# Kernel optimization log

Measured on AMD Instinct MI355X. Metric: run time of the kernel, lower is better.

Reference implementation:

```python
import math
import jax, jax.numpy as jnp
import numpy as np
from jax.scipy.special import xlogy, gammaln


def get_positional_embed(seq_len, feature_size):
    # Enformer-style relative positional basis over distances [-(L-1), L-1].
    distances = jnp.arange(-seq_len + 1, seq_len, dtype=jnp.float32)  # [2L-1]
    n = feature_size // 6
    absd = jnp.abs(distances)[:, None]  # [2L-1, 1]

    # exponential basis
    max_range = math.log(seq_len) / math.log(2.0)
    half_life = 2.0 ** jnp.linspace(3.0, max_range, n)  # [n]
    feat_exp = jnp.exp(-math.log(2.0) / half_life[None, :] * absd)

    # central mask basis
    center_widths = 2.0 ** jnp.arange(1, n + 1, dtype=jnp.float32) - 1.0
    feat_cm = (center_widths[None, :] > absd).astype(jnp.float32)

    # gamma pdf basis
    stddev = seq_len / (2.0 * n)
    start_mean = seq_len / n
    mean = jnp.linspace(start_mean, float(seq_len), n)[None, :]
    conc = (mean / stddev) ** 2
    rate = mean / stddev ** 2
    log_unnorm = xlogy(conc - 1.0, absd) - rate * absd
    log_norm = gammaln(conc) - conc * jnp.log(rate)
    probs = jnp.exp(log_unnorm - log_norm) + 1e-8
    feat_gamma = probs / jnp.max(probs, axis=-1, keepdims=True)

    emb = jnp.concatenate([feat_exp, feat_cm, feat_gamma], axis=-1)  # [2L-1, 3n]
    emb = jnp.concatenate([emb, jnp.sign(distances)[:, None] * emb], axis=-1)  # [2L-1, 6n]
    return emb


def relative_shift(x):
    # x: [B, H, Q, 2K-1] -> [B, H, Q, K]
    b, h, t1, t2m1 = x.shape
    x = jnp.pad(x, ((0, 0), (0, 0), (0, 0), (1, 0)))  # [B,H,Q,2K]
    t2 = t2m1 + 1
    x = x.reshape(b, h, t2, t1)
    x = x[:, :, 1:, :]
    x = x.reshape(b, h, t1, t2 - 1)
    return x[..., : (t2 + 1) // 2]


def setup_inputs() -> dict:
    key = jax.random.key(0)
    ks = jax.random.split(key, 9)
    B, L, D = 2, 1024, 1024
    H, Dk, Dv = 8, 128, 128
    R = 192  # n_rel_pos_features
    sq = math.sqrt(2.0 / (D + Dk))
    sv = math.sqrt(2.0 / (D + Dv))
    return {
        "q": jax.random.normal(ks[0], (B, L, D), jnp.float32),
        "w_qs": jax.random.normal(ks[1], (D, H * Dk), jnp.float32) * sq,
        "w_ks": jax.random.normal(ks[2], (D, H * Dk), jnp.float32) * sq,
        "w_vs": jax.random.normal(ks[3], (D, H * Dv), jnp.float32) * sv,
        "w_rel_pos_k": jax.random.normal(ks[4], (R, H * Dk), jnp.float32) * 0.05,
        "rel_embed_bias": jax.random.normal(ks[5], (1, H, 1, Dk), jnp.float32),
        "rel_pos_bias": jax.random.normal(ks[6], (1, H, 1, Dk), jnp.float32),
        "w_out": jax.random.normal(ks[7], (H * Dv, D), jnp.float32) * 0.02,
        "b_out": jax.random.normal(ks[8], (D,), jnp.float32) * 0.02,
    }


def reference(q, w_qs, w_ks, w_vs, w_rel_pos_k, rel_embed_bias, rel_pos_bias, w_out, b_out):
    B, L, _ = q.shape
    H, Dk = rel_embed_bias.shape[1], rel_embed_bias.shape[3]
    Dv = w_vs.shape[1] // H
    scale = Dk ** (-0.5)

    Q = (q @ w_qs).reshape(B, L, H, Dk).transpose(0, 2, 1, 3) * scale  # [B,H,L,Dk]
    K = (q @ w_ks).reshape(B, L, H, Dk).transpose(0, 2, 1, 3)
    V = (q @ w_vs).reshape(B, L, H, Dv).transpose(0, 2, 1, 3)

    attn = jnp.einsum('bnqd,bnkd->bnqk', Q + rel_embed_bias, K)

    positions = get_positional_embed(L, w_rel_pos_k.shape[0])  # [2L-1, R]
    rel_k = (positions @ w_rel_pos_k).reshape(-1, H, Dk).transpose(1, 0, 2)  # [H,2L-1,Dk]
    attn_pos = jnp.einsum('bnqd,nkd->bnqk', Q + rel_pos_bias, rel_k)  # [B,H,L,2L-1]
    attn_pos = relative_shift(attn_pos)  # [B,H,L,L]

    a = jax.nn.softmax(attn + attn_pos, axis=-1)
    out = jnp.einsum('bnqk,bnkd->bnqd', a, V)
    out = out.transpose(0, 2, 1, 3).reshape(B, L, H * Dv)
    return out @ w_out + b_out
```

## Files before the change

### kernel.cpp

```cpp
#include <hip/hip_runtime.h>
#include <hip/hip_fp16.h>

typedef __attribute__((ext_vector_type(8))) _Float16 f16x8;
typedef __attribute__((ext_vector_type(4))) float f32x4;

#define MFMA16(a, b, c) __builtin_amdgcn_mfma_f32_16x16x32_f16((a), (b), (c), 0, 0, 0)

__device__ __forceinline__ unsigned short f2h(float f) {
  __half h = __float2half(f);
  return __half_as_ushort(h);
}

__device__ __forceinline__ void gll16(const void* g, void* l) {
  __builtin_amdgcn_global_load_lds(
      (const __attribute__((address_space(1))) unsigned int*)g,
      (__attribute__((address_space(3))) unsigned int*)l, 16, 0, 0);
}

__global__ void cvt_f16_kernel(const float* __restrict__ X, unsigned short* __restrict__ Y) {
  size_t i = ((size_t)blockIdx.x * blockDim.x + threadIdx.x) * 4;
  float4 v = *reinterpret_cast<const float4*>(X + i);
  ushort4 o;
  o.x = f2h(v.x); o.y = f2h(v.y); o.z = f2h(v.z); o.w = f2h(v.w);
  *reinterpret_cast<ushort4*>(Y + i) = o;
}

__global__ void transpose_w4_kernel(const float* __restrict__ W0, const float* __restrict__ W1,
                                    const float* __restrict__ W2, const float* __restrict__ W3,
                                    unsigned short* __restrict__ T0, unsigned short* __restrict__ T1,
                                    unsigned short* __restrict__ T2, unsigned short* __restrict__ T3) {
  __shared__ float tile[32][33];
  int z = blockIdx.z;
  const float* W = (z == 0) ? W0 : ((z == 1) ? W1 : ((z == 2) ? W2 : W3));
  unsigned short* WT = (z == 0) ? T0 : ((z == 1) ? T1 : ((z == 2) ? T2 : T3));
  int c0 = blockIdx.x * 32, r0 = blockIdx.y * 32;
  int tx = threadIdx.x, ty = threadIdx.y;
#pragma unroll
  for (int i = 0; i < 32; i += 8)
    tile[ty + i][tx] = W[(size_t)(r0 + ty + i) * 1024 + c0 + tx];
  __syncthreads();
#pragma unroll
  for (int i = 0; i < 32; i += 8)
    WT[(size_t)(c0 + ty + i) * 1024 + r0 + tx] = f2h(tile[tx][ty + i]);
}

__global__ void transpose_wr_kernel(const float* __restrict__ W, unsigned short* __restrict__ WT) {
  __shared__ float tile[32][33];
  int c0 = blockIdx.x * 32, r0 = blockIdx.y * 32;
  int tx = threadIdx.x, ty = threadIdx.y;
#pragma unroll
  for (int i = 0; i < 32; i += 8)
    tile[ty + i][tx] = W[(size_t)(r0 + ty + i) * 1024 + c0 + tx];
  __syncthreads();
#pragma unroll
  for (int i = 0; i < 32; i += 8)
    WT[(size_t)(c0 + ty + i) * 192 + r0 + tx] = f2h(tile[tx][ty + i]);
}

__global__ void posembed_kernel(unsigned short* __restrict__ pos) {
  int grp = (blockIdx.x * blockDim.x + threadIdx.x) >> 5;
  int j = threadIdx.x & 31;
  if (grp >= 2048) return;
  unsigned short* row = pos + (size_t)grp * 192;
  if (grp == 2047) {
#pragma unroll
    for (int t = 0; t < 6; ++t) row[t * 32 + j] = 0;
    return;
  }
  float dist = (float)grp - 1023.0f;
  float absd = fabsf(dist);
  float jp = (float)(j + 1);
  float hl = exp2f(3.0f + (float)j * (7.0f / 31.0f));
  float fe = exp2f(-absd / hl);
  float cw = exp2f(jp) - 1.0f;
  float fc = (cw > absd) ? 1.0f : 0.0f;
  float conc = 4.0f * jp * jp;
  float rate = 0.125f * jp;
  float lu = (conc - 1.0f) * logf(absd) - rate * absd;
  float ln_ = lgammaf(conc) - conc * logf(rate);
  float p = expf(lu - ln_) + 1e-8f;
  float mp = p;
#pragma unroll
  for (int off = 16; off >= 1; off >>= 1) mp = fmaxf(mp, __shfl_xor(mp, off));
  float gm = p / mp;
  unsigned short e = f2h(fe), c = f2h(fc), gg = f2h(gm);
  row[j] = e; row[32 + j] = c; row[64 + j] = gg;
  unsigned short se, sc, sg;
  if (dist > 0.0f)      { se = e; sc = c; sg = gg; }
  else if (dist < 0.0f) { se = (unsigned short)(e ^ 0x8000u);
                          sc = (unsigned short)(c ^ 0x8000u);
                          sg = (unsigned short)(gg ^ 0x8000u); }
  else                  { se = 0; sc = 0; sg = 0; }
  row[96 + j] = se; row[128 + j] = sc; row[160 + j] = sg;
}

__global__ __launch_bounds__(256) void gemm16_kernel(
    const unsigned short* __restrict__ A,
    const unsigned short* __restrict__ BT0, const unsigned short* __restrict__ BT1,
    const unsigned short* __restrict__ BT2,
    unsigned short* __restrict__ D0, unsigned short* __restrict__ D1,
    unsigned short* __restrict__ D2,
    float* __restrict__ C32, const float* __restrict__ bias,
    int M, int N, int K) {
  __shared__ unsigned short As[128][64];
  __shared__ unsigned short Bs[128][64];
  const unsigned short* BT = (blockIdx.z == 0) ? BT0 : ((blockIdx.z == 1) ? BT1 : BT2);
  unsigned short* D = (blockIdx.z == 0) ? D0 : ((blockIdx.z == 1) ? D1 : D2);

  int tid = threadIdx.x, wave = tid >> 6, lane = tid & 63;
  int g = lane >> 4, r16 = lane & 15;
  int wr = wave >> 1, wc = wave & 1;
  int m0 = blockIdx.x * 128, n0 = blockIdx.y * 128;
  int srow = wave * 32 + (lane >> 3);
  int scb = lane & 7;

  f32x4 acc[4][4] = {};

  for (int k0 = 0; k0 < K; k0 += 64) {
    __syncthreads();
#pragma unroll
    for (int i = 0; i < 4; ++i) {
      int row = srow + i * 8;
      int cb = scb ^ (row & 7);
      gll16(A + (size_t)(m0 + row) * K + k0 + cb * 8, &As[row][scb * 8]);
      gll16(BT + (size_t)(n0 + row) * K + k0 + cb * 8, &Bs[row][scb * 8]);
    }
    asm volatile("s_waitcnt vmcnt(0)" ::: "memory");
    __syncthreads();

    f16x8 af[2][4], bfr[2][4];
#pragma unroll
    for (int kf = 0; kf < 2; ++kf) {
#pragma unroll
      for (int mt = 0; mt < 4; ++mt) {
        int R = wr * 64 + mt * 16 + r16;
        af[kf][mt] = *reinterpret_cast<const f16x8*>(&As[R][(((kf * 4 + g)) ^ (R & 7)) * 8]);
      }
#pragma unroll
      for (int nt = 0; nt < 4; ++nt) {
        int R = wc * 64 + nt * 16 + r16;
        bfr[kf][nt] = *reinterpret_cast<const f16x8*>(&Bs[R][(((kf * 4 + g)) ^ (R & 7)) * 8]);
      }
    }
#pragma unroll
    for (int kf = 0; kf < 2; ++kf)
#pragma unroll
      for (int mt = 0; mt < 4; ++mt)
#pragma unroll
        for (int nt = 0; nt < 4; ++nt)
          acc[mt][nt] = MFMA16(af[kf][mt], bfr[kf][nt], acc[mt][nt]);
  }

#pragma unroll
  for (int nt = 0; nt < 4; ++nt) {
    int col = n0 + wc * 64 + nt * 16 + r16;
    float bv = (C32 && bias) ? bias[col] : 0.0f;
#pragma unroll
    for (int mt = 0; mt < 4; ++mt) {
      int rowb = m0 + wr * 64 + mt * 16 + g * 4;
      if (C32) {
#pragma unroll
        for (int rg = 0; rg < 4; ++rg)
          C32[(size_t)(rowb + rg) * N + col] = acc[mt][nt][rg] + bv;
      } else {
#pragma unroll
        for (int rg = 0; rg < 4; ++rg)
          D[(size_t)(rowb + rg) * N + col] = f2h(acc[mt][nt][rg]);
      }
    }
  }
}

__global__ void vt_prep_kernel(const unsigned short* __restrict__ Vh, unsigned short* __restrict__ Vt) {
  __shared__ unsigned short tile[32][34];
  int bh = blockIdx.z;
  int b = bh >> 3, h = bh & 7;
  int l0 = blockIdx.x * 32, n0 = blockIdx.y * 32;
  int tx = threadIdx.x, ty = threadIdx.y;
#pragma unroll
  for (int i = 0; i < 32; i += 8)
    tile[ty + i][tx] = Vh[(size_t)(b * 1024 + l0 + ty + i) * 1024 + h * 128 + n0 + tx];
  __syncthreads();
#pragma unroll
  for (int i = 0; i < 32; i += 8)
    Vt[(size_t)bh * 131072 + (size_t)(n0 + ty + i) * 1024 + l0 + tx] = tile[tx][ty + i];
}

__global__ __launch_bounds__(256) void attn_kernel(
    const unsigned short* __restrict__ Qh, const unsigned short* __restrict__ Kh,
    const unsigned short* __restrict__ Vt, const unsigned short* __restrict__ relkh,
    const float* __restrict__ eb, const float* __restrict__ pb,
    unsigned short* __restrict__ Opart, float* __restrict__ mlpart) {
  __shared__ unsigned short Ks[2][32 * 128];
  __shared__ unsigned short Rs[128 * 128];
  __shared__ unsigned short Vs[2][128][40];
  __shared__ unsigned short Ps[4][16][42];

  int tid = threadIdx.x;
  int wave = tid >> 6, lane = tid & 63;
  int g = lane >> 4, r16 = lane & 15;
  int ks = blockIdx.y;
  int bh = blockIdx.z;
  int b = bh >> 3, h = bh & 7;
  int q0 = blockIdx.x * 64;
  int q0w = q0 + wave * 16;
  const float scale = 0.0883883476483184f;

  f16x8 qa[4], qbv[4];
  {
    int qrow = b * 1024 + q0w + r16;
    const unsigned short* qp = Qh + (size_t)qrow * 1024 + h * 128;
    const float* ebp = eb + h * 128;
    const float* pbp = pb + h * 128;
#pragma unroll
    for (int kf = 0; kf < 4; ++kf) {
      int dbase = kf * 32 + g * 8;
      uint4 qv = *reinterpret_cast<const uint4*>(qp + dbase);
      const __half* hv = reinterpret_cast<const __half*>(&qv);
      float4 e0 = *reinterpret_cast<const float4*>(ebp + dbase);
      float4 e1 = *reinterpret_cast<const float4*>(ebp + dbase + 4);
      float4 c0 = *reinterpret_cast<const float4*>(pbp + dbase);
      float4 c1 = *reinterpret_cast<const float4*>(pbp + dbase + 4);
      float ev[8] = {e0.x, e0.y, e0.z, e0.w, e1.x, e1.y, e1.z, e1.w};
      float bv[8] = {c0.x, c0.y, c0.z, c0.w, c1.x, c1.y, c1.z, c1.w};
      unsigned short ta[8], tb[8];
#pragma unroll
      for (int i = 0; i < 8; ++i) {
        float s = __half2float(hv[i]) * scale;
        ta[i] = f2h(s + ev[i]);
        tb[i] = f2h(s + bv[i]);
      }
      qa[kf] = *reinterpret_cast<f16x8*>(ta);
      qbv[kf] = *reinterpret_cast<f16x8*>(tb);
    }
  }

  float m_run[4], l_part[4];
#pragma unroll
  for (int rg = 0; rg < 4; ++rg) { m_run[rg] = -1e30f; l_part[rg] = 0.0f; }
  f32x4 o_acc[8] = {};

  const unsigned short* KB = Kh + ((size_t)b * 1024) * 1024 + h * 128;
  const unsigned short* VB = Vt + (size_t)bh * 131072;
  const unsigned short* RB = relkh + h * 128;
  int wb = 48 - wave * 16;

  const int t0 = ks * 16, t1 = t0 + 16;
  const int rb0 = 960 + t0 * 32 - q0;

  uint4 va, vb2;
#pragma unroll
  for (int i = 0; i < 2; ++i) {
    int j = i * 256 + tid;
    int row = j >> 4, s = j & 15, c = s ^ (row & 7);
    gll16(KB + (size_t)(t0 * 32 + row) * 1024 + c * 8, &Ks[t0 & 1][(row * 16 + s) * 8]);
  }
#pragma unroll
  for (int i = 0; i < 6; ++i) {
    int j = i * 256 + tid;
    int row = rb0 + (j >> 4);
    int s = j & 15, c = s ^ (row & 7);
    gll16(RB + (size_t)row * 1024 + c * 8, &Rs[(((row & 127) * 16) + s) * 8]);
  }
  {
    const unsigned short* src = VB + (size_t)(tid >> 1) * 1024 + t0 * 32 + (tid & 1) * 16;
    va = *reinterpret_cast<const uint4*>(src);
    vb2 = *reinterpret_cast<const uint4*>(src + 8);
  }

  for (int t = t0; t < t1; ++t) {
    int cur = t & 1;
    asm volatile("s_waitcnt vmcnt(0)" ::: "memory");
    {
      int rr = tid >> 1, cc = (tid & 1) * 16;
      *reinterpret_cast<uint4*>(&Vs[cur][rr][cc]) = va;
      *reinterpret_cast<uint4*>(&Vs[cur][rr][cc + 8]) = vb2;
    }
    __syncthreads();

    if (t + 1 < t1) {
      int nk0 = (t + 1) * 32;
#pragma unroll
      for (int i = 0; i < 2; ++i) {
        int j = i * 256 + tid;
        int row = j >> 4, s = j & 15, c = s ^ (row & 7);
        gll16(KB + (size_t)(nk0 + row) * 1024 + c * 8, &Ks[(t + 1) & 1][(row * 16 + s) * 8]);
      }
      int rnew = rb0 + 96 + (t - t0) * 32;
#pragma unroll
      for (int i = 0; i < 2; ++i) {
        int j = i * 256 + tid;
        int row = rnew + (j >> 4);
        int s = j & 15, c = s ^ (row & 7);
        gll16(RB + (size_t)row * 1024 + c * 8, &Rs[(((row & 127) * 16) + s) * 8]);
      }
      const unsigned short* src = VB + (size_t)(tid >> 1) * 1024 + nk0 + (tid & 1) * 16;
      va = *reinterpret_cast<const uint4*>(src);
      vb2 = *reinterpret_cast<const uint4*>(src + 8);
    }

    int k0 = t * 32;
    int rbt = rb0 + (t - t0) * 32;
    f32x4 s0 = {0.f, 0.f, 0.f, 0.f}, s1 = {0.f, 0.f, 0.f, 0.f};
    f32x4 w0 = {0.f, 0.f, 0.f, 0.f}, w1 = {0.f, 0.f, 0.f, 0.f}, w2 = {0.f, 0.f, 0.f, 0.f};
#pragma unroll
    for (int kf = 0; kf < 4; ++kf) {
      int sl = kf * 4 + g;
      int x = sl ^ (r16 & 7);
      f16x8 kb0 = *reinterpret_cast<const f16x8*>(&Ks[cur][(r16 * 16 + x) * 8]);
      f16x8 kb1 = *reinterpret_cast<const f16x8*>(&Ks[cur][((16 + r16) * 16 + x) * 8]);
      s0 = MFMA16(qa[kf], kb0, s0);
      s1 = MFMA16(qa[kf], kb1, s1);
      int R0 = rbt + wb + r16, R1 = R0 + 16, R2 = R0 + 32;
      f16x8 rb_0 = *reinterpret_cast<const f16x8*>(&Rs[((R0 & 127) * 16 + (sl ^ (R0 & 7))) * 8]);
      f16x8 rb_1 = *reinterpret_cast<const f16x8*>(&Rs[((R1 & 127) * 16 + (sl ^ (R1 & 7))) * 8]);
      f16x8 rb_2 = *reinterpret_cast<const f16x8*>(&Rs[((R2 & 127) * 16 + (sl ^ (R2 & 7))) * 8]);
      w0 = MFMA16(qbv[kf], rb_0, w0);
      w1 = MFMA16(qbv[kf], rb_1, w1);
      w2 = MFMA16(qbv[kf], rb_2, w2);
    }

    float sv[2][4];
#pragma unroll
    for (int rg = 0; rg < 4; ++rg) {
      int qp = g * 4 + rg;
      int idx = r16 + 15 - qp;
      int srcl = (lane & 48) | (idx & 15);
      float a0 = __shfl(w0[rg], srcl);
      float a1 = __shfl(w1[rg], srcl);
      float a2 = __shfl(w2[rg], srcl);
      bool lo = idx < 16;
      sv[0][rg] = s0[rg] + (lo ? a0 : a1);
      sv[1][rg] = s1[rg] + (lo ? a1 : a2);
    }

    float d = -1e30f;
#pragma unroll
    for (int rg = 0; rg < 4; ++rg)
      d = fmaxf(d, fmaxf(sv[0][rg], sv[1][rg]) - m_run[rg]);
    if (!__all(d <= 8.0f)) {
#pragma unroll
      for (int rg = 0; rg < 4; ++rg) {
        float mx = fmaxf(sv[0][rg], sv[1][rg]);
#pragma unroll
        for (int off = 8; off >= 1; off >>= 1) mx = fmaxf(mx, __shfl_xor(mx, off));
        float mnew = fmaxf(m_run[rg], mx);
        float scl = __expf(m_run[rg] - mnew);
        l_part[rg] *= scl;
#pragma unroll
        for (int nf = 0; nf < 8; ++nf) o_acc[nf][rg] *= scl;
        m_run[rg] = mnew;
      }
    }
#pragma unroll
    for (int rg = 0; rg < 4; ++rg) {
      float e0 = __expf(sv[0][rg] - m_run[rg]);
      float e1 = __expf(sv[1][rg] - m_run[rg]);
      l_part[rg] += e0 + e1;
      Ps[wave][g * 4 + rg][r16] = f2h(e0);
      Ps[wave][g * 4 + rg][16 + r16] = f2h(e1);
    }
    f16x8 pf = *reinterpret_cast<const f16x8*>(&Ps[wave][r16][g * 8]);
#pragma unroll
    for (int nf = 0; nf < 8; ++nf) {
      f16x8 vb = *reinterpret_cast<const f16x8*>(&Vs[cur][nf * 16 + r16][g * 8]);
      o_acc[nf] = MFMA16(pf, vb, o_acc[nf]);
    }
  }

  float l_run[4];
#pragma unroll
  for (int rg = 0; rg < 4; ++rg) {
    float rs = l_part[rg];
#pragma unroll
    for (int off = 8; off >= 1; off >>= 1) rs += __shfl_xor(rs, off);
    l_run[rg] = rs;
  }

  size_t slice = (size_t)(ks * 16 + bh);
#pragma unroll
  for (int rg = 0; rg < 4; ++rg) {
    unsigned short* op = Opart + (slice * 1024 + q0w + g * 4 + rg) * 128;
#pragma unroll
    for (int nf = 0; nf < 8; ++nf) op[nf * 16 + r16] = f2h(o_acc[nf][rg]);
  }
  if (r16 == 0) {
#pragma unroll
    for (int rg = 0; rg < 4; ++rg) {
      float2 ml = {m_run[rg], l_run[rg]};
      *reinterpret_cast<float2*>(mlpart + (slice * 1024 + q0w + g * 4 + rg) * 2) = ml;
    }
  }
}

__global__ void combine_kernel(const unsigned short* __restrict__ Opart,
                               const float* __restrict__ mlpart,
                               unsigned short* __restrict__ attnO) {
  int idx = blockIdx.x * 256 + threadIdx.x;
  int d4 = (idx & 31) * 4;
  int qq = (idx >> 5) & 1023;
  int bh = idx >> 15;
  float2 ml[2];
  float m = -1e30f;
#pragma unroll
  for (int s = 0; s < 2; ++s) {
    ml[s] = *reinterpret_cast<const float2*>(mlpart + (((size_t)(s * 16 + bh)) * 1024 + qq) * 2);
    m = fmaxf(m, ml[s].x);
  }
  float num0 = 0.f, num1 = 0.f, num2 = 0.f, num3 = 0.f, den = 0.f;
#pragma unroll
  for (int s = 0; s < 2; ++s) {
    float w = __expf(ml[s].x - m);
    den += w * ml[s].y;
    ushort4 ov = *reinterpret_cast<const ushort4*>(
        Opart + (((size_t)(s * 16 + bh)) * 1024 + qq) * 128 + d4);
    num0 += w * __half2float(__ushort_as_half(ov.x));
    num1 += w * __half2float(__ushort_as_half(ov.y));
    num2 += w * __half2float(__ushort_as_half(ov.z));
    num3 += w * __half2float(__ushort_as_half(ov.w));
  }
  float inv = 1.0f / den;
  ushort4 o;
  o.x = f2h(num0 * inv); o.y = f2h(num1 * inv);
  o.z = f2h(num2 * inv); o.w = f2h(num3 * inv);
  int b = bh >> 3, h = bh & 7;
  *reinterpret_cast<ushort4*>(attnO + ((size_t)(b * 1024 + qq)) * 1024 + h * 128 + d4) = o;
}

extern "C" void kernel_launch(void* const* d_in, const int* in_sizes, int n_in,
                              void* d_out, int out_size, void* d_ws, size_t ws_size,
                              hipStream_t stream) {
  const float* q      = (const float*)d_in[0];
  const float* w_qs   = (const float*)d_in[1];
  const float* w_ks   = (const float*)d_in[2];
  const float* w_vs   = (const float*)d_in[3];
  const float* w_rel  = (const float*)d_in[4];
  const float* ebias  = (const float*)d_in[5];
  const float* pbias  = (const float*)d_in[6];
  const float* w_out  = (const float*)d_in[7];
  const float* b_out  = (const float*)d_in[8];
  float* out = (float*)d_out;

  char* ws = (char*)d_ws;
  const size_t MB = 1u << 20;
  unsigned short* Xh    = (unsigned short*)(ws + 0 * MB);
  unsigned short* WqsT  = (unsigned short*)(ws + 4 * MB);
  unsigned short* WksT  = (unsigned short*)(ws + 6 * MB);
  unsigned short* WvsT  = (unsigned short*)(ws + 8 * MB);
  unsigned short* WoutT = (unsigned short*)(ws + 10 * MB);
  unsigned short* WrelT = (unsigned short*)(ws + 12 * MB);
  unsigned short* pos   = (unsigned short*)(ws + 13 * MB);
  unsigned short* Qh    = (unsigned short*)(ws + 14 * MB);
  unsigned short* Kh    = (unsigned short*)(ws + 18 * MB);
  unsigned short* Vh    = (unsigned short*)(ws + 22 * MB);
  unsigned short* relkh = (unsigned short*)(ws + 26 * MB);
  unsigned short* Vt    = (unsigned short*)(ws + 30 * MB);
  unsigned short* attnO = (unsigned short*)(ws + 34 * MB);
  unsigned short* Opart = (unsigned short*)(ws + 38 * MB);
  float* mlpart         = (float*)(ws + 50 * MB);

  cvt_f16_kernel<<<2048, 256, 0, stream>>>(q, Xh);
  transpose_w4_kernel<<<dim3(32, 32, 4), dim3(32, 8), 0, stream>>>(
      w_qs, w_ks, w_vs, w_out, WqsT, WksT, WvsT, WoutT);
  transpose_wr_kernel<<<dim3(32, 6), dim3(32, 8), 0, stream>>>(w_rel, WrelT);
  posembed_kernel<<<256, 256, 0, stream>>>(pos);

  gemm16_kernel<<<dim3(16, 8, 3), 256, 0, stream>>>(Xh, WqsT, WksT, WvsT,
                                                    Qh, Kh, Vh,
                                                    nullptr, nullptr, 2048, 1024, 1024);
  gemm16_kernel<<<dim3(16, 8, 1), 256, 0, stream>>>(pos, WrelT, WrelT, WrelT,
                                                    relkh, relkh, relkh,
                                                    nullptr, nullptr, 2048, 1024, 192);

  vt_prep_kernel<<<dim3(32, 4, 16), dim3(32, 8), 0, stream>>>(Vh, Vt);

  attn_kernel<<<dim3(16, 2, 16), 256, 0, stream>>>(Qh, Kh, Vt, relkh, ebias, pbias,
                                                   Opart, mlpart);
  combine_kernel<<<2048, 256, 0, stream>>>(Opart, mlpart, attnO);

  gemm16_kernel<<<dim3(16, 8, 1), 256, 0, stream>>>(attnO, WoutT, WoutT, WoutT,
                                                    nullptr, nullptr, nullptr,
                                                    out, b_out, 2048, 1024, 1024);
}
```

Before: 118.7 us.

## Merge rel-pos GEMM into QKV launch, split-K output GEMM, swizzle attention blocks

```diff
diff --git a/kernel.cpp b/kernel.cpp
--- a/kernel.cpp
+++ b/kernel.cpp
@@ -95,17 +95,20 @@
 }
 
 __global__ __launch_bounds__(256) void gemm16_kernel(
-    const unsigned short* __restrict__ A,
+    const unsigned short* __restrict__ A, const unsigned short* __restrict__ A3,
     const unsigned short* __restrict__ BT0, const unsigned short* __restrict__ BT1,
-    const unsigned short* __restrict__ BT2,
+    const unsigned short* __restrict__ BT2, const unsigned short* __restrict__ BT3,
     unsigned short* __restrict__ D0, unsigned short* __restrict__ D1,
-    unsigned short* __restrict__ D2,
-    float* __restrict__ C32, const float* __restrict__ bias,
-    int M, int N, int K) {
+    unsigned short* __restrict__ D2, unsigned short* __restrict__ D3,
+    int Kmain, int K3) {
   __shared__ unsigned short As[128][64];
   __shared__ unsigned short Bs[128][64];
-  const unsigned short* BT = (blockIdx.z == 0) ? BT0 : ((blockIdx.z == 1) ? BT1 : BT2);
-  unsigned short* D = (blockIdx.z == 0) ? D0 : ((blockIdx.z == 1) ? D1 : D2);
+  int z = blockIdx.z;
+  const unsigned short* Az = (z == 3) ? A3 : A;
+  const unsigned short* BT = (z == 0) ? BT0 : ((z == 1) ? BT1 : ((z == 2) ? BT2 : BT3));
+  unsigned short* D = (z == 0) ? D0 : ((z == 1) ? D1 : ((z == 2) ? D2 : D3));
+  int K = (z == 3) ? K3 : Kmain;
+  const int N = 1024;
 
   int tid = threadIdx.x, wave = tid >> 6, lane = tid & 63;
   int g = lane >> 4, r16 = lane & 15;
@@ -122,7 +125,7 @@
     for (int i = 0; i < 4; ++i) {
       int row = srow + i * 8;
       int cb = scb ^ (row & 7);
-      gll16(A + (size_t)(m0 + row) * K + k0 + cb * 8, &As[row][scb * 8]);
+      gll16(Az + (size_t)(m0 + row) * K + k0 + cb * 8, &As[row][scb * 8]);
       gll16(BT + (size_t)(n0 + row) * K + k0 + cb * 8, &Bs[row][scb * 8]);
     }
     asm volatile("s_waitcnt vmcnt(0)" ::: "memory");
@@ -154,19 +157,82 @@
 #pragma unroll
   for (int nt = 0; nt < 4; ++nt) {
     int col = n0 + wc * 64 + nt * 16 + r16;
-    float bv = (C32 && bias) ? bias[col] : 0.0f;
 #pragma unroll
     for (int mt = 0; mt < 4; ++mt) {
       int rowb = m0 + wr * 64 + mt * 16 + g * 4;
-      if (C32) {
-#pragma unroll
-        for (int rg = 0; rg < 4; ++rg)
-          C32[(size_t)(rowb + rg) * N + col] = acc[mt][nt][rg] + bv;
-      } else {
-#pragma unroll
-        for (int rg = 0; rg < 4; ++rg)
-          D[(size_t)(rowb + rg) * N + col] = f2h(acc[mt][nt][rg]);
-      }
+#pragma unroll
+      for (int rg = 0; rg < 4; ++rg)
+        D[(size_t)(rowb + rg) * N + col] = f2h(acc[mt][nt][rg]);
+    }
+  }
+}
+
+__global__ void bias_init_kernel(const float* __restrict__ b, float* __restrict__ out) {
+  size_t i = ((size_t)blockIdx.x * 256 + threadIdx.x) * 4;
+  float4 bv = *reinterpret_cast<const float4*>(b + (i & 1023));
+  *reinterpret_cast<float4*>(out + i) = bv;
+}
+
+__global__ __launch_bounds__(256) void gemm16_atomic_kernel(
+    const unsigned short* __restrict__ A, const unsigned short* __restrict__ BT,
+    float* __restrict__ C) {
+  __shared__ unsigned short As[128][64];
+  __shared__ unsigned short Bs[128][64];
+  const int N = 1024, K = 1024;
+  int tid = threadIdx.x, wave = tid >> 6, lane = tid & 63;
+  int g = lane >> 4, r16 = lane & 15;
+  int wr = wave >> 1, wc = wave & 1;
+  int m0 = blockIdx.x * 128, n0 = blockIdx.y * 128;
+  int kb = blockIdx.z * 512;
+  int srow = wave * 32 + (lane >> 3);
+  int scb = lane & 7;
+
+  f32x4 acc[4][4] = {};
+
+  for (int k0 = kb; k0 < kb + 512; k0 += 64) {
+    __syncthreads();
+#pragma unroll
+    for (int i = 0; i < 4; ++i) {
+      int row = srow + i * 8;
+      int cb = scb ^ (row & 7);
+      gll16(A + (size_t)(m0 + row) * K + k0 + cb * 8, &As[row][scb * 8]);
+      gll16(BT + (size_t)(n0 + row) * K + k0 + cb * 8, &Bs[row][scb * 8]);
+    }
+    asm volatile("s_waitcnt vmcnt(0)" ::: "memory");
+    __syncthreads();
+
+    f16x8 af[2][4], bfr[2][4];
+#pragma unroll
+    for (int kf = 0; kf < 2; ++kf) {
+#pragma unroll
+      for (int mt = 0; mt < 4; ++mt) {
+        int R = wr * 64 + mt * 16 + r16;
+        af[kf][mt] = *reinterpret_cast<const f16x8*>(&As[R][(((kf * 4 + g)) ^ (R & 7)) * 8]);
+      }
+#pragma unroll
+      for (int nt = 0; nt < 4; ++nt) {
+        int R = wc * 64 + nt * 16 + r16;
+        bfr[kf][nt] = *reinterpret_cast<const f16x8*>(&Bs[R][(((kf * 4 + g)) ^ (R & 7)) * 8]);
+      }
+    }
+#pragma unroll
+    for (int kf = 0; kf < 2; ++kf)
+#pragma unroll
+      for (int mt = 0; mt < 4; ++mt)
+#pragma unroll
+        for (int nt = 0; nt < 4; ++nt)
+          acc[mt][nt] = MFMA16(af[kf][mt], bfr[kf][nt], acc[mt][nt]);
+  }
+
+#pragma unroll
+  for (int nt = 0; nt < 4; ++nt) {
+    int col = n0 + wc * 64 + nt * 16 + r16;
+#pragma unroll
+    for (int mt = 0; mt < 4; ++mt) {
+      int rowb = m0 + wr * 64 + mt * 16 + g * 4;
+#pragma unroll
+      for (int rg = 0; rg < 4; ++rg)
+        atomicAdd(&C[(size_t)(rowb + rg) * N + col], acc[mt][nt][rg]);
     }
   }
 }
@@ -194,15 +260,18 @@
   __shared__ unsigned short Ks[2][32 * 128];
   __shared__ unsigned short Rs[128 * 128];
   __shared__ unsigned short Vs[2][128][40];
-  __shared__ unsigned short Ps[4][16][42];
+  __shared__ unsigned short Ps[4][16][40];
 
   int tid = threadIdx.x;
   int wave = tid >> 6, lane = tid & 63;
   int g = lane >> 4, r16 = lane & 15;
-  int ks = blockIdx.y;
-  int bh = blockIdx.z;
+
+  int lin = blockIdx.x + 16 * (blockIdx.y + 2 * blockIdx.z);
+  int swz = (lin & 7) * 64 + (lin >> 3);
+  int ks = (swz >> 4) & 1;
+  int bh = swz >> 5;
   int b = bh >> 3, h = bh & 7;
-  int q0 = blockIdx.x * 64;
+  int q0 = (swz & 15) * 64;
   int q0w = q0 + wave * 16;
   const float scale = 0.0883883476483184f;
 
@@ -299,7 +368,6 @@
       vb2 = *reinterpret_cast<const uint4*>(src + 8);
     }
 
-    int k0 = t * 32;
     int rbt = rb0 + (t - t0) * 32;
     f32x4 s0 = {0.f, 0.f, 0.f, 0.f}, s1 = {0.f, 0.f, 0.f, 0.f};
     f32x4 w0 = {0.f, 0.f, 0.f, 0.f}, w1 = {0.f, 0.f, 0.f, 0.f}, w2 = {0.f, 0.f, 0.f, 0.f};
@@ -465,12 +533,8 @@
   transpose_wr_kernel<<<dim3(32, 6), dim3(32, 8), 0, stream>>>(w_rel, WrelT);
   posembed_kernel<<<256, 256, 0, stream>>>(pos);
 
-  gemm16_kernel<<<dim3(16, 8, 3), 256, 0, stream>>>(Xh, WqsT, WksT, WvsT,
-                                                    Qh, Kh, Vh,
-                                                    nullptr, nullptr, 2048, 1024, 1024);
-  gemm16_kernel<<<dim3(16, 8, 1), 256, 0, stream>>>(pos, WrelT, WrelT, WrelT,
-                                                    relkh, relkh, relkh,
-                                                    nullptr, nullptr, 2048, 1024, 192);
+  gemm16_kernel<<<dim3(16, 8, 4), 256, 0, stream>>>(
+      Xh, pos, WqsT, WksT, WvsT, WrelT, Qh, Kh, Vh, relkh, 1024, 192);
 
   vt_prep_kernel<<<dim3(32, 4, 16), dim3(32, 8), 0, stream>>>(Vh, Vt);
 
@@ -478,7 +542,6 @@
                                                    Opart, mlpart);
   combine_kernel<<<2048, 256, 0, stream>>>(Opart, mlpart, attnO);
 
-  gemm16_kernel<<<dim3(16, 8, 1), 256, 0, stream>>>(attnO, WoutT, WoutT, WoutT,
-                                                    nullptr, nullptr, nullptr,
-                                                    out, b_out, 2048, 1024, 1024);
-}
+  bias_init_kernel<<<2048, 256, 0, stream>>>(b_out, out);
+  gemm16_atomic_kernel<<<dim3(16, 8, 2), 256, 0, stream>>>(attnO, WoutT, out);
+}
```

Result: faster. 111.5 us (-6.0%).
